# Optimization experiments

Measured on AMD Instinct MI355X. Metric: run time of the kernel, lower is better.

## Reference

```python
import jax, jax.numpy as jnp
import numpy as np

D_MODEL = 1024
D_INNER = 2048   # expand * d_model
D_STATE = 16
DT_RANK = 64     # ceil(d_model / 16)
D_CONV = 4
L = 2048
EPS = 1e-5


def setup_inputs() -> dict:
    key = jax.random.key(0)
    ks = jax.random.split(key, 8)
    sc = lambda k, shape: jax.random.normal(k, shape, jnp.float32) * 0.02
    A = jnp.tile(jnp.arange(1, D_STATE + 1, dtype=jnp.float32), (D_INNER, 1))
    return {
        "x": jax.random.normal(ks[0], (L, D_MODEL), jnp.float32),
        "W_in": sc(ks[1], (D_MODEL, 2 * D_INNER)),          # in_proj (no bias)
        "W_conv": sc(ks[2], (D_CONV, D_INNER)),             # depthwise conv kernel
        "b_conv": jnp.zeros((D_INNER,), jnp.float32),
        "W_x": sc(ks[3], (D_INNER, DT_RANK + 2 * D_STATE)), # x_proj (no bias)
        "W_dt": sc(ks[4], (DT_RANK, D_INNER)),
        "b_dt": jnp.zeros((D_INNER,), jnp.float32),
        "A_log": jnp.log(A),
        "D": jnp.ones((D_INNER,), jnp.float32),
        "W_out": sc(ks[5], (D_INNER, D_MODEL)),             # out_proj (no bias)
        "ln_scale": jnp.ones((D_MODEL,), jnp.float32),
        "ln_bias": jnp.zeros((D_MODEL,), jnp.float32),
        "drop_key": 0,  # unused: training=False -> DropPath is identity
    }


def reference(x, W_in, W_conv, b_conv, W_x, W_dt, b_dt, A_log, D, W_out,
              ln_scale, ln_bias, drop_key):
    l = x.shape[0]
    # LayerNorm (flax default: mean/var over features)
    mu = jnp.mean(x, axis=-1, keepdims=True)
    var = jnp.mean(jnp.square(x), axis=-1, keepdims=True) - jnp.square(mu)
    xn = (x - mu) * jax.lax.rsqrt(var + EPS) * ln_scale + ln_bias

    # MambaBlock
    xr = xn @ W_in                         # (l, 2*d_inner)
    u, res = xr[:, :D_INNER], xr[:, D_INNER:]

    # causal depthwise conv: pad left d_conv-1, take first l outputs
    up = jnp.pad(u, ((D_CONV - 1, 0), (0, 0)))
    uc = b_conv + sum(up[k:k + l] * W_conv[k] for k in range(D_CONV))
    u2 = jax.nn.silu(uc)                   # (l, d_inner)

    # SSM params (input-dependent)
    x_dbl = u2 @ W_x                       # (l, dt_rank + 2n)
    dt = x_dbl[:, :DT_RANK]
    B = x_dbl[:, DT_RANK:DT_RANK + D_STATE]
    C = x_dbl[:, DT_RANK + D_STATE:]
    delta = jax.nn.softplus(dt @ W_dt + b_dt)   # (l, d_inner)
    A = -jnp.exp(A_log)                         # (d_inner, n)

    dA = jnp.exp(jnp.einsum('ld,dn->ldn', delta, A))   # (l, d_inner, n)
    dBu = jnp.einsum('ld,ln->ldn', delta * u2, B)       # (l, d_inner, n)

    def step(h, inp):
        dA_t, dBu_t, C_t = inp
        h = dA_t * h + dBu_t               # (d_inner, n)
        return h, h @ C_t                  # y_t: (d_inner,)

    h0 = jnp.zeros((D_INNER, D_STATE), dtype=u2.dtype)
    _, ys = jax.lax.scan(step, h0, (dA, dBu, C))
    y = ys + u2 * D                        # (l, d_inner)

    y = y * jax.nn.silu(res)
    out = y @ W_out                        # (l, d_model)
    return out + x                         # residual (DropPath identity in eval)
```

## Files before the change

### kernel.cpp

```cpp
#include <hip/hip_runtime.h>
#include <math.h>

#define L_SEQ 2048
#define DM 1024
#define DI 2048
#define DS 16
#define DTR 64
#define EPS 1e-5f
#define NSEG 16
#define SEGLEN 128

typedef float f32x4 __attribute__((ext_vector_type(4)));
typedef __bf16 bf16x8 __attribute__((ext_vector_type(8)));
typedef _Float16 h16x4 __attribute__((ext_vector_type(4)));

static __device__ __forceinline__ unsigned short f2bf(float f) {
  union { float f; unsigned u; } v; v.f = f;
  unsigned r = v.u + 0x7fffu + ((v.u >> 16) & 1u);
  return (unsigned short)(r >> 16);
}
static __device__ __forceinline__ float bf2f(unsigned short s) {
  union { unsigned u; float f; } v; v.u = ((unsigned)s) << 16;
  return v.f;
}

static __device__ __forceinline__ void gload16(const void* g, void* l) {
  __builtin_amdgcn_global_load_lds(
      (__attribute__((address_space(1))) void*)(unsigned long long)(g),
      (__attribute__((address_space(3))) void*)(unsigned)(unsigned long long)(l),
      16, 0, 0);
}

__global__ __launch_bounds__(256) void ln_kernel(const float* __restrict__ x,
                                                 const float* __restrict__ sc,
                                                 const float* __restrict__ bi,
                                                 unsigned short* __restrict__ xnb) {
  int row = blockIdx.x;
  int t = threadIdx.x;
  float4 xv = ((const float4*)(x + (size_t)row * DM))[t];
  float s  = xv.x + xv.y + xv.z + xv.w;
  float s2 = xv.x*xv.x + xv.y*xv.y + xv.z*xv.z + xv.w*xv.w;
  #pragma unroll
  for (int m = 32; m >= 1; m >>= 1) {
    s  += __shfl_xor(s, m);
    s2 += __shfl_xor(s2, m);
  }
  __shared__ float red[8];
  int wid = t >> 6, lane = t & 63;
  if (lane == 0) { red[wid] = s; red[4 + wid] = s2; }
  __syncthreads();
  s  = red[0] + red[1] + red[2] + red[3];
  s2 = red[4] + red[5] + red[6] + red[7];
  float mu = s * (1.f / DM);
  float var = s2 * (1.f / DM) - mu * mu;
  float rs = rsqrtf(var + EPS);
  float4 sc4 = ((const float4*)sc)[t];
  float4 bi4 = ((const float4*)bi)[t];
  ushort4 ob;
  ob.x = f2bf((xv.x - mu) * rs * sc4.x + bi4.x);
  ob.y = f2bf((xv.y - mu) * rs * sc4.y + bi4.y);
  ob.z = f2bf((xv.z - mu) * rs * sc4.z + bi4.z);
  ob.w = f2bf((xv.w - mu) * rs * sc4.w + bi4.w);
  *(ushort4*)&xnb[(size_t)row * DM + t * 4] = ob;
}

__global__ __launch_bounds__(256) void trans_bf16(
    const float* __restrict__ W, unsigned short* __restrict__ Wt, int K, int N)
{
  __shared__ unsigned short s[64][80];
  int n0 = blockIdx.x * 64, k0 = blockIdx.y * 64;
  int tid = threadIdx.x;
  #pragma unroll
  for (int p = 0; p < 4; ++p) {
    int i = p * 16 + (tid >> 4);
    int j = (tid & 15) * 4;
    float4 w = *(const float4*)&W[(size_t)(k0 + i) * N + n0 + j];
    s[j + 0][i] = f2bf(w.x); s[j + 1][i] = f2bf(w.y);
    s[j + 2][i] = f2bf(w.z); s[j + 3][i] = f2bf(w.w);
  }
  __syncthreads();
  #pragma unroll
  for (int q = 0; q < 2; ++q) {
    int n = q * 32 + (tid >> 3);
    int i8 = (tid & 7) * 8;
    *(int4*)&Wt[(size_t)(n0 + n) * K + k0 + i8] = *(const int4*)&s[n][i8];
  }
}

__global__ __launch_bounds__(256) void transpose_b16(
    const unsigned short* __restrict__ in, unsigned short* __restrict__ out,
    int R, int C)
{
  __shared__ unsigned short s[64][72];
  int c0 = blockIdx.x * 64, r0 = blockIdx.y * 64;
  int tid = threadIdx.x;
  #pragma unroll
  for (int p = 0; p < 2; ++p) {
    int r = p * 32 + (tid >> 3);
    int c = (tid & 7) * 8;
    *(int4*)&s[r][c] = *(const int4*)&in[(size_t)(r0 + r) * C + c0 + c];
  }
  __syncthreads();
  #pragma unroll
  for (int p = 0; p < 2; ++p) {
    int c = p * 32 + (tid >> 3);
    int r = (tid & 7) * 8;
    ushort4 a, b;
    a.x = s[r + 0][c]; a.y = s[r + 1][c]; a.z = s[r + 2][c]; a.w = s[r + 3][c];
    b.x = s[r + 4][c]; b.y = s[r + 5][c]; b.z = s[r + 6][c]; b.w = s[r + 7][c];
    *(ushort4*)&out[(size_t)(c0 + c) * R + r0 + r] = a;
    *(ushort4*)&out[(size_t)(c0 + c) * R + r0 + r + 4] = b;
  }
}

__global__ __launch_bounds__(256) void trans_wx(
    const float* __restrict__ Wx, unsigned short* __restrict__ Wxt)
{
  int i = blockIdx.x * 256 + threadIdx.x;
  int n = i >> 11, k = i & 2047;
  Wxt[i] = (n < 96) ? f2bf(Wx[(size_t)k * 96 + n]) : (unsigned short)0;
}

template<int BM, int BN, int EPI, int OUTB, int SPLITK>
__global__ __launch_bounds__(256) void gemm2(
    const unsigned short* __restrict__ A, int lda,
    const unsigned short* __restrict__ Bt, int ldb,
    void* __restrict__ Cv, int ldc,
    int M, int N, int K,
    const float* __restrict__ bias)
{
  constexpr int WM = BM / 2, WN = BN / 2;
  constexpr int FM = WM / 16, FN = WN / 16;
  __shared__ __align__(16) unsigned short smA[BM * 64];
  __shared__ __align__(16) unsigned short smB[BN * 64];

  int nwg = gridDim.x * gridDim.y;
  int bid = blockIdx.y * gridDim.x + blockIdx.x;
  if ((nwg & 7) == 0) {
    int cpx = nwg >> 3;
    bid = (bid & 7) * cpx + (bid >> 3);
  }
  int bx = bid % gridDim.x;
  int by = bid / gridDim.x;
  int m0 = by * BM, n0 = bx * BN;

  int tid = threadIdx.x;
  int lane = tid & 63, wid = tid >> 6;
  int wm = wid >> 1, wn = wid & 1;

  int kb = blockIdx.z * (K / SPLITK);
  int nt = (K / SPLITK) / 64;

  int rs = lane >> 3;
  int cs = (lane & 7) * 8;

  f32x4 acc[FM][FN];
  #pragma unroll
  for (int m = 0; m < FM; ++m)
    #pragma unroll
    for (int n = 0; n < FN; ++n) acc[m][n] = (f32x4){0.f, 0.f, 0.f, 0.f};

  for (int kt = 0; kt < nt; ++kt) {
    __syncthreads();
    #pragma unroll
    for (int i = 0; i < BM / 32; ++i) {
      int chunk = wid * (BM / 32) + i;
      gload16(A + (size_t)(m0 + chunk * 8 + rs) * lda + kb + kt * 64 + cs,
              (char*)smA + chunk * 1024);
    }
    #pragma unroll
    for (int i = 0; i < BN / 32; ++i) {
      int chunk = wid * (BN / 32) + i;
      gload16(Bt + (size_t)(n0 + chunk * 8 + rs) * ldb + kb + kt * 64 + cs,
              (char*)smB + chunk * 1024);
    }
    __syncthreads();

    #pragma unroll
    for (int kk = 0; kk < 2; ++kk) {
      bf16x8 aF[FM], bF[FN];
      #pragma unroll
      for (int m = 0; m < FM; ++m) {
        int r = wm * WM + m * 16 + (lane & 15);
        aF[m] = *(const bf16x8*)((const char*)smA + r * 128 + kk * 64 + (lane >> 4) * 16);
      }
      #pragma unroll
      for (int n = 0; n < FN; ++n) {
        int r = wn * WN + n * 16 + (lane & 15);
        bF[n] = *(const bf16x8*)((const char*)smB + r * 128 + kk * 64 + (lane >> 4) * 16);
      }
      #pragma unroll
      for (int m = 0; m < FM; ++m)
        #pragma unroll
        for (int n = 0; n < FN; ++n)
          acc[m][n] = __builtin_amdgcn_mfma_f32_16x16x32_bf16(
              aF[m], bF[n], acc[m][n], 0, 0, 0);
    }
  }

  float* Cf = (float*)Cv + (size_t)blockIdx.z * M * ldc;
  unsigned short* Cb = (unsigned short*)Cv;
  int cm = (lane >> 4) * 4, cn = lane & 15;
  #pragma unroll
  for (int m = 0; m < FM; ++m)
    #pragma unroll
    for (int n = 0; n < FN; ++n) {
      int col = n0 + wn * WN + n * 16 + cn;
      #pragma unroll
      for (int r = 0; r < 4; ++r) {
        int row = m0 + wm * WM + m * 16 + cm + r;
        float v = acc[m][n][r];
        if (EPI == 1) {
          float w = v + bias[row];
          v = (w > 20.f) ? w : log1pf(__expf(w));
        }
        if (OUTB) Cb[(size_t)row * ldc + col] = f2bf(v);
        else      Cf[(size_t)row * ldc + col] = v;
      }
    }
}

__global__ __launch_bounds__(256) void xdbl_reduce(
    const float* __restrict__ part, unsigned short* __restrict__ xdbl)
{
  int i = (blockIdx.x * 256 + threadIdx.x) * 4;
  const int SL = 2048 * 128;
  float4 s = *(const float4*)&part[i];
  #pragma unroll
  for (int z = 1; z < 16; ++z) {
    float4 p = *(const float4*)&part[(size_t)z * SL + i];
    s.x += p.x; s.y += p.y; s.z += p.z; s.w += p.w;
  }
  ushort4 ob;
  ob.x = f2bf(s.x); ob.y = f2bf(s.y); ob.z = f2bf(s.z); ob.w = f2bf(s.w);
  *(ushort4*)&xdbl[i] = ob;
}

__global__ __launch_bounds__(256) void out_reduce(
    const float* __restrict__ part, const float* __restrict__ x,
    float* __restrict__ out)
{
  int i = (blockIdx.x * 256 + threadIdx.x) * 4;
  const int SL = 2048 * 1024;
  float4 a = *(const float4*)&part[i];
  float4 b = *(const float4*)&part[SL + i];
  float4 r = *(const float4*)&x[i];
  float4 o;
  o.x = a.x + b.x + r.x; o.y = a.y + b.y + r.y;
  o.z = a.z + b.z + r.z; o.w = a.w + b.w + r.w;
  *(float4*)&out[i] = o;
}

__global__ __launch_bounds__(256) void conv_silu_kernel(
    const unsigned short* __restrict__ xrT,
    const float* __restrict__ Wc, const float* __restrict__ bc,
    unsigned short* __restrict__ u2T)
{
  int d = blockIdx.x;
  int l0 = blockIdx.y * 1024 + threadIdx.x * 4;
  const unsigned short* ur = xrT + (size_t)d * L_SEQ;
  float w0 = Wc[0 * DI + d], w1 = Wc[1 * DI + d];
  float w2 = Wc[2 * DI + d], w3 = Wc[3 * DI + d];
  float b = bc[d];
  ushort4 v0 = *(const ushort4*)&ur[l0];
  ushort4 vm; vm.x = vm.y = vm.z = vm.w = 0;
  if (l0 > 0) vm = *(const ushort4*)&ur[l0 - 4];
  float um3 = bf2f(vm.y), um2 = bf2f(vm.z), um1 = bf2f(vm.w);
  float x0 = bf2f(v0.x), x1 = bf2f(v0.y), x2 = bf2f(v0.z), x3 = bf2f(v0.w);
  float y0 = b + w0 * um3 + w1 * um2 + w2 * um1 + w3 * x0;
  float y1 = b + w0 * um2 + w1 * um1 + w2 * x0  + w3 * x1;
  float y2 = b + w0 * um1 + w1 * x0  + w2 * x1  + w3 * x2;
  float y3 = b + w0 * x0  + w1 * x1  + w2 * x2  + w3 * x3;
  ushort4 ob;
  ob.x = f2bf(y0 / (1.f + __expf(-y0)));
  ob.y = f2bf(y1 / (1.f + __expf(-y1)));
  ob.z = f2bf(y2 / (1.f + __expf(-y2)));
  ob.w = f2bf(y3 / (1.f + __expf(-y3)));
  *(ushort4*)&u2T[(size_t)d * L_SEQ + l0] = ob;
}


__global__ __launch_bounds__(64) void scan_pass1(
    const unsigned short* __restrict__ deltaT, const unsigned short* __restrict__ u2T,
    const unsigned short* __restrict__ xdbl,
    const float* __restrict__ A_log,
    float* __restrict__ hend, float* __restrict__ aprod)
{
  int t = threadIdx.x;
  int ch = t >> 4, n = t & 15;
  int li = (t & 15) * 4;
  int d0 = blockIdx.x * 4, d = d0 + ch;
  int s = blockIdx.y;
  int base = s * SEGLEN;

  __shared__ __align__(16) float sdT[4][68], suT[4][68], sBT[16][68];

  float An = -__expf(A_log[d * DS + n]);
  float h = 0.f, P = 1.f;

  ushort4 rdu, ru, rB[4];
  auto LOAD = [&](int c0) {
    rdu = *(const ushort4*)&deltaT[(size_t)d * L_SEQ + c0 + li];
    ru  = *(const ushort4*)&u2T[(size_t)d * L_SEQ + c0 + li];
    #pragma unroll
    for (int r = 0; r < 4; ++r) {
      int ll = c0 + (t >> 2) + r * 16;
      rB[r] = *(const ushort4*)&xdbl[(size_t)ll * 128 + 64 + (t & 3) * 4];
    }
  };

  LOAD(base);
  for (int cc = 0; cc < 2; ++cc) {
    __syncthreads();
    sdT[ch][li + 0] = bf2f(rdu.x); sdT[ch][li + 1] = bf2f(rdu.y);
    sdT[ch][li + 2] = bf2f(rdu.z); sdT[ch][li + 3] = bf2f(rdu.w);
    suT[ch][li + 0] = bf2f(ru.x);  suT[ch][li + 1] = bf2f(ru.y);
    suT[ch][li + 2] = bf2f(ru.z);  suT[ch][li + 3] = bf2f(ru.w);
    #pragma unroll
    for (int r = 0; r < 4; ++r) {
      int ll = (t >> 2) + r * 16;
      int nb = (t & 3) * 4;
      sBT[nb + 0][ll] = bf2f(rB[r].x); sBT[nb + 1][ll] = bf2f(rB[r].y);
      sBT[nb + 2][ll] = bf2f(rB[r].z); sBT[nb + 3][ll] = bf2f(rB[r].w);
    }
    if (cc == 0) LOAD(base + 64);
    __syncthreads();

    #pragma unroll
    for (int g = 0; g < 64; g += 4) {
      float4 dl4 = *(const float4*)&sdT[ch][g];
      float4 ul4 = *(const float4*)&suT[ch][g];
      float4 Bn4 = *(const float4*)&sBT[n][g];
      float dl[4] = {dl4.x, dl4.y, dl4.z, dl4.w};
      float ul[4] = {ul4.x, ul4.y, ul4.z, ul4.w};
      float Bn[4] = {Bn4.x, Bn4.y, Bn4.z, Bn4.w};
      #pragma unroll
      for (int i = 0; i < 4; ++i) {
        float dA = __expf(dl[i] * An);
        P *= dA;
        h = dA * h + (dl[i] * ul[i]) * Bn[i];
      }
    }
  }
  size_t idx = (size_t)s * (DI * DS) + d0 * DS + t;
  hend[idx]  = h;
  aprod[idx] = P;
}

__global__ __launch_bounds__(64) void scan_pass3(
    const unsigned short* __restrict__ deltaT, const unsigned short* __restrict__ u2T,
    const unsigned short* __restrict__ resT,
    const unsigned short* __restrict__ xdbl,
    const float* __restrict__ A_log, const float* __restrict__ Dp,
    const float* __restrict__ hend, const float* __restrict__ aprod,
    unsigned short* __restrict__ ybT)
{
  int t = threadIdx.x;
  int ch = t >> 4, n = t & 15;
  int li = (t & 15) * 4;
  int d0 = blockIdx.x * 4, d = d0 + ch;
  int s = blockIdx.y;
  int base = s * SEGLEN;

  __shared__ __align__(16) float sdT[4][68], suT[4][68];
  __shared__ __align__(16) float sBT[16][68], sCT[16][68];
  __shared__ __align__(16) _Float16 svh[64][68];

  float An = -__expf(A_log[d * DS + n]);
  float Dd = Dp[d];

  float h = 0.f;
  int fi = d0 * DS + t;
  for (int k = 0; k < s; ++k)
    h = aprod[(size_t)k * (DI * DS) + fi] * h + hend[(size_t)k * (DI * DS) + fi];

  ushort4 rdu, ru, rB[4], rC[4];
  auto LOAD = [&](int c0) {
    rdu = *(const ushort4*)&deltaT[(size_t)d * L_SEQ + c0 + li];
    ru  = *(const ushort4*)&u2T[(size_t)d * L_SEQ + c0 + li];
    #pragma unroll
    for (int r = 0; r < 4; ++r) {
      int ll = c0 + (t >> 2) + r * 16;
      int n4 = (t & 3) * 4;
      rB[r] = *(const ushort4*)&xdbl[(size_t)ll * 128 + 64 + n4];
      rC[r] = *(const ushort4*)&xdbl[(size_t)ll * 128 + 80 + n4];
    }
  };

  LOAD(base);
  for (int cc = 0; cc < 2; ++cc) {
    int c0 = base + cc * 64;
    __syncthreads();
    sdT[ch][li + 0] = bf2f(rdu.x); sdT[ch][li + 1] = bf2f(rdu.y);
    sdT[ch][li + 2] = bf2f(rdu.z); sdT[ch][li + 3] = bf2f(rdu.w);
    suT[ch][li + 0] = bf2f(ru.x);  suT[ch][li + 1] = bf2f(ru.y);
    suT[ch][li + 2] = bf2f(ru.z);  suT[ch][li + 3] = bf2f(ru.w);
    #pragma unroll
    for (int r = 0; r < 4; ++r) {
      int ll = (t >> 2) + r * 16;
      int nb = (t & 3) * 4;
      sBT[nb + 0][ll] = bf2f(rB[r].x); sBT[nb + 1][ll] = bf2f(rB[r].y);
      sBT[nb + 2][ll] = bf2f(rB[r].z); sBT[nb + 3][ll] = bf2f(rB[r].w);
      sCT[nb + 0][ll] = bf2f(rC[r].x); sCT[nb + 1][ll] = bf2f(rC[r].y);
      sCT[nb + 2][ll] = bf2f(rC[r].z); sCT[nb + 3][ll] = bf2f(rC[r].w);
    }
    if (cc == 0) LOAD(base + 64);
    __syncthreads();

    #pragma unroll
    for (int g = 0; g < 64; g += 4) {
      float4 dl4 = *(const float4*)&sdT[ch][g];
      float4 ul4 = *(const float4*)&suT[ch][g];
      float4 Bn4 = *(const float4*)&sBT[n][g];
      float4 Cn4 = *(const float4*)&sCT[n][g];
      float dl[4] = {dl4.x, dl4.y, dl4.z, dl4.w};
      float ul[4] = {ul4.x, ul4.y, ul4.z, ul4.w};
      float Bn[4] = {Bn4.x, Bn4.y, Bn4.z, Bn4.w};
      float Cn[4] = {Cn4.x, Cn4.y, Cn4.z, Cn4.w};
      #pragma unroll
      for (int i = 0; i < 4; ++i) {
        float dA = __expf(dl[i] * An);
        h = dA * h + (dl[i] * ul[i]) * Bn[i];
        float vv = h * Cn[i];
        if (n == 0) vv += ul[i] * Dd;
        svh[g + i][t] = (_Float16)vv;
      }
    }
    __syncthreads();

    #pragma unroll
    for (int r = 0; r < 4; ++r) {
      int ll = (t >> 2) + r * 16;
      int c2 = t & 3;
      const h16x4* p = (const h16x4*)&svh[ll][c2 * 16];
      h16x4 a = p[0], b = p[1], c = p[2], e = p[3];
      float sA = ((float)a.x + (float)a.y) + ((float)a.z + (float)a.w);
      float sB = ((float)b.x + (float)b.y) + ((float)b.z + (float)b.w);
      float sC = ((float)c.x + (float)c.y) + ((float)c.z + (float)c.w);
      float sE = ((float)e.x + (float)e.y) + ((float)e.z + (float)e.w);
      float sum = (sA + sB) + (sC + sE);
      float rv = bf2f(resT[(size_t)(d0 + c2) * L_SEQ + c0 + ll]);
      float sig = 1.f / (1.f + __expf(-rv));
      ybT[(size_t)(d0 + c2) * L_SEQ + c0 + ll] = f2bf(sum * rv * sig);
    }
  }
}

extern "C" void kernel_launch(void* const* d_in, const int* in_sizes, int n_in,
                              void* d_out, int out_size, void* d_ws, size_t ws_size,
                              hipStream_t stream)
{
  const float* x      = (const float*)d_in[0];
  const float* W_in   = (const float*)d_in[1];
  const float* W_conv = (const float*)d_in[2];
  const float* b_conv = (const float*)d_in[3];
  const float* W_x    = (const float*)d_in[4];
  const float* W_dt   = (const float*)d_in[5];
  const float* b_dt   = (const float*)d_in[6];
  const float* A_log  = (const float*)d_in[7];
  const float* Dp     = (const float*)d_in[8];
  const float* W_out  = (const float*)d_in[9];
  const float* ln_s   = (const float*)d_in[10];
  const float* ln_b   = (const float*)d_in[11];

  char* ws = (char*)d_ws;
  const size_t MB = 1u << 20;
  unsigned short* xnb    = (unsigned short*)(ws);
  unsigned short* xrT    = (unsigned short*)(ws + 4 * MB);
  unsigned short* u2T    = (unsigned short*)(ws + 20 * MB);
  unsigned short* u2b    = (unsigned short*)(ws + 28 * MB);
  float*          hend   = (float*)(ws + 28 * MB);
  float*          aprod  = (float*)(ws + 30 * MB);
  unsigned short* xdbl   = (unsigned short*)(ws + 36 * MB);
  unsigned short* Wxt    = (unsigned short*)(ws + 36 * MB + 512 * 1024);
  unsigned short* Wdt_t  = (unsigned short*)(ws + 37 * MB);
  unsigned short* deltaTb= (unsigned short*)(ws + 38 * MB);
  unsigned short* Wtin   = (unsigned short*)(ws + 38 * MB);
  float*          part   = (float*)(ws + 46 * MB);
  unsigned short* ybT    = (unsigned short*)(ws + 54 * MB);
  unsigned short* yb     = (unsigned short*)(ws + 4 * MB);
  unsigned short* Wtout  = xnb;
  const unsigned short* resT = xrT + (size_t)DI * L_SEQ;

  ln_kernel<<<L_SEQ, 256, 0, stream>>>(x, ln_s, ln_b, xnb);

  trans_bf16<<<dim3((2 * DI) / 64, DM / 64), 256, 0, stream>>>(W_in, Wtin, DM, 2 * DI);

  gemm2<64, 128, 0, 1, 1><<<dim3(L_SEQ / 128, (2 * DI) / 64), 256, 0, stream>>>(
      Wtin, DM, xnb, DM, xrT, L_SEQ, 2 * DI, L_SEQ, DM, nullptr);

  conv_silu_kernel<<<dim3(DI, 2), 256, 0, stream>>>(xrT, W_conv, b_conv, u2T);

  transpose_b16<<<dim3(L_SEQ / 64, DI / 64), 256, 0, stream>>>(u2T, u2b, DI, L_SEQ);

  trans_wx<<<(128 * 2048) / 256, 256, 0, stream>>>(W_x, Wxt);

  gemm2<64, 128, 0, 0, 16><<<dim3(1, L_SEQ / 64, 16), 256, 0, stream>>>(
      u2b, DI, Wxt, DI, part, 128, L_SEQ, 128, DI, nullptr);

  xdbl_reduce<<<(L_SEQ * 128) / 1024, 256, 0, stream>>>(part, xdbl);

  trans_bf16<<<dim3(DI / 64, DTR / 64), 256, 0, stream>>>(W_dt, Wdt_t, DTR, DI);

  gemm2<64, 128, 1, 1, 1><<<dim3(L_SEQ / 128, DI / 64), 256, 0, stream>>>(
      Wdt_t, DTR, xdbl, 128, deltaTb, L_SEQ, DI, L_SEQ, DTR, b_dt);

  trans_bf16<<<dim3(DM / 64, DI / 64), 256, 0, stream>>>(W_out, Wtout, DI, DM);

  scan_pass1<<<dim3(DI / 4, NSEG), 64, 0, stream>>>(
      deltaTb, u2T, xdbl, A_log, hend, aprod);

  scan_pass3<<<dim3(DI / 4, NSEG), 64, 0, stream>>>(
      deltaTb, u2T, resT, xdbl, A_log, Dp, hend, aprod, ybT);

  transpose_b16<<<dim3(L_SEQ / 64, DI / 64), 256, 0, stream>>>(ybT, yb, DI, L_SEQ);

  gemm2<64, 64, 0, 0, 2><<<dim3(DM / 64, L_SEQ / 64, 2), 256, 0, stream>>>(
      yb, DI, Wtout, DI, part, DM, L_SEQ, DM, DI, nullptr);

  out_reduce<<<(L_SEQ * DM) / 1024, 256, 0, stream>>>(part, x, (float*)d_out);
}
```

Measured before the change: 189.0 us.

## Widen scan blocks to 8 channels, precompute delta*u, skip last segment pass1

Both scan kernels now run 128-thread blocks covering 8 channels instead of 4, so each block loads the shared B/C tiles once for twice as many channels. The delta*u product is computed once per element while staging to shared memory rather than per state lane. The D skip term moves from the inner loop into the final reduction, and pass1 no longer launches for the last segment, whose end state is never consumed. The wider shared staging buffer and re-read of u2 add some shared memory and global traffic per block.

Result: faster. 185.2 us (-2.0%).

```diff
diff --git a/kernel.cpp b/kernel.cpp
--- a/kernel.cpp
+++ b/kernel.cpp
@@ -12,7 +12,7 @@
 
 typedef float f32x4 __attribute__((ext_vector_type(4)));
 typedef __bf16 bf16x8 __attribute__((ext_vector_type(8)));
-typedef _Float16 h16x4 __attribute__((ext_vector_type(4)));
+typedef _Float16 h16x2 __attribute__((ext_vector_type(2)));
 
 static __device__ __forceinline__ unsigned short f2bf(float f) {
   union { float f; unsigned u; } v; v.f = f;
@@ -280,7 +280,7 @@
 }
 
 
-__global__ __launch_bounds__(64) void scan_pass1(
+__global__ __launch_bounds__(128) void scan_pass1(
     const unsigned short* __restrict__ deltaT, const unsigned short* __restrict__ u2T,
     const unsigned short* __restrict__ xdbl,
     const float* __restrict__ A_log,
@@ -289,39 +289,40 @@
   int t = threadIdx.x;
   int ch = t >> 4, n = t & 15;
   int li = (t & 15) * 4;
-  int d0 = blockIdx.x * 4, d = d0 + ch;
+  int d0 = blockIdx.x * 8, d = d0 + ch;
   int s = blockIdx.y;
   int base = s * SEGLEN;
 
-  __shared__ __align__(16) float sdT[4][68], suT[4][68], sBT[16][68];
+  __shared__ __align__(16) float sdT[8][68], suT[8][68], sBT[16][68];
 
   float An = -__expf(A_log[d * DS + n]);
   float h = 0.f, P = 1.f;
 
-  ushort4 rdu, ru, rB[4];
+  ushort4 rdu, ru, rB[2];
   auto LOAD = [&](int c0) {
     rdu = *(const ushort4*)&deltaT[(size_t)d * L_SEQ + c0 + li];
     ru  = *(const ushort4*)&u2T[(size_t)d * L_SEQ + c0 + li];
     #pragma unroll
-    for (int r = 0; r < 4; ++r) {
-      int ll = c0 + (t >> 2) + r * 16;
-      rB[r] = *(const ushort4*)&xdbl[(size_t)ll * 128 + 64 + (t & 3) * 4];
+    for (int q = 0; q < 2; ++q) {
+      int ll = c0 + (t >> 2) + q * 32;
+      rB[q] = *(const ushort4*)&xdbl[(size_t)ll * 128 + 64 + (t & 3) * 4];
     }
   };
 
   LOAD(base);
   for (int cc = 0; cc < 2; ++cc) {
     __syncthreads();
-    sdT[ch][li + 0] = bf2f(rdu.x); sdT[ch][li + 1] = bf2f(rdu.y);
-    sdT[ch][li + 2] = bf2f(rdu.z); sdT[ch][li + 3] = bf2f(rdu.w);
-    suT[ch][li + 0] = bf2f(ru.x);  suT[ch][li + 1] = bf2f(ru.y);
-    suT[ch][li + 2] = bf2f(ru.z);  suT[ch][li + 3] = bf2f(ru.w);
-    #pragma unroll
-    for (int r = 0; r < 4; ++r) {
-      int ll = (t >> 2) + r * 16;
+    float d0v = bf2f(rdu.x), d1v = bf2f(rdu.y), d2v = bf2f(rdu.z), d3v = bf2f(rdu.w);
+    sdT[ch][li + 0] = d0v; sdT[ch][li + 1] = d1v;
+    sdT[ch][li + 2] = d2v; sdT[ch][li + 3] = d3v;
+    suT[ch][li + 0] = d0v * bf2f(ru.x); suT[ch][li + 1] = d1v * bf2f(ru.y);
+    suT[ch][li + 2] = d2v * bf2f(ru.z); suT[ch][li + 3] = d3v * bf2f(ru.w);
+    #pragma unroll
+    for (int q = 0; q < 2; ++q) {
+      int ll = (t >> 2) + q * 32;
       int nb = (t & 3) * 4;
-      sBT[nb + 0][ll] = bf2f(rB[r].x); sBT[nb + 1][ll] = bf2f(rB[r].y);
-      sBT[nb + 2][ll] = bf2f(rB[r].z); sBT[nb + 3][ll] = bf2f(rB[r].w);
+      sBT[nb + 0][ll] = bf2f(rB[q].x); sBT[nb + 1][ll] = bf2f(rB[q].y);
+      sBT[nb + 2][ll] = bf2f(rB[q].z); sBT[nb + 3][ll] = bf2f(rB[q].w);
     }
     if (cc == 0) LOAD(base + 64);
     __syncthreads();
@@ -329,16 +330,16 @@
     #pragma unroll
     for (int g = 0; g < 64; g += 4) {
       float4 dl4 = *(const float4*)&sdT[ch][g];
-      float4 ul4 = *(const float4*)&suT[ch][g];
+      float4 du4 = *(const float4*)&suT[ch][g];
       float4 Bn4 = *(const float4*)&sBT[n][g];
       float dl[4] = {dl4.x, dl4.y, dl4.z, dl4.w};
-      float ul[4] = {ul4.x, ul4.y, ul4.z, ul4.w};
+      float du[4] = {du4.x, du4.y, du4.z, du4.w};
       float Bn[4] = {Bn4.x, Bn4.y, Bn4.z, Bn4.w};
       #pragma unroll
       for (int i = 0; i < 4; ++i) {
         float dA = __expf(dl[i] * An);
         P *= dA;
-        h = dA * h + (dl[i] * ul[i]) * Bn[i];
+        h = dA * h + du[i] * Bn[i];
       }
     }
   }
@@ -347,7 +348,7 @@
   aprod[idx] = P;
 }
 
-__global__ __launch_bounds__(64) void scan_pass3(
+__global__ __launch_bounds__(128) void scan_pass3(
     const unsigned short* __restrict__ deltaT, const unsigned short* __restrict__ u2T,
     const unsigned short* __restrict__ resT,
     const unsigned short* __restrict__ xdbl,
@@ -358,32 +359,31 @@
   int t = threadIdx.x;
   int ch = t >> 4, n = t & 15;
   int li = (t & 15) * 4;
-  int d0 = blockIdx.x * 4, d = d0 + ch;
+  int d0 = blockIdx.x * 8, d = d0 + ch;
   int s = blockIdx.y;
   int base = s * SEGLEN;
 
-  __shared__ __align__(16) float sdT[4][68], suT[4][68];
+  __shared__ __align__(16) float sdT[8][68], suT[8][68];
   __shared__ __align__(16) float sBT[16][68], sCT[16][68];
-  __shared__ __align__(16) _Float16 svh[64][68];
+  __shared__ __align__(4) _Float16 svh[64][134];
 
   float An = -__expf(A_log[d * DS + n]);
-  float Dd = Dp[d];
 
   float h = 0.f;
   int fi = d0 * DS + t;
   for (int k = 0; k < s; ++k)
     h = aprod[(size_t)k * (DI * DS) + fi] * h + hend[(size_t)k * (DI * DS) + fi];
 
-  ushort4 rdu, ru, rB[4], rC[4];
+  ushort4 rdu, ru, rB[2], rC[2];
   auto LOAD = [&](int c0) {
     rdu = *(const ushort4*)&deltaT[(size_t)d * L_SEQ + c0 + li];
     ru  = *(const ushort4*)&u2T[(size_t)d * L_SEQ + c0 + li];
     #pragma unroll
-    for (int r = 0; r < 4; ++r) {
-      int ll = c0 + (t >> 2) + r * 16;
+    for (int q = 0; q < 2; ++q) {
+      int ll = c0 + (t >> 2) + q * 32;
       int n4 = (t & 3) * 4;
-      rB[r] = *(const ushort4*)&xdbl[(size_t)ll * 128 + 64 + n4];
-      rC[r] = *(const ushort4*)&xdbl[(size_t)ll * 128 + 80 + n4];
+      rB[q] = *(const ushort4*)&xdbl[(size_t)ll * 128 + 64 + n4];
+      rC[q] = *(const ushort4*)&xdbl[(size_t)ll * 128 + 80 + n4];
     }
   };
 
@@ -391,18 +391,19 @@
   for (int cc = 0; cc < 2; ++cc) {
     int c0 = base + cc * 64;
     __syncthreads();
-    sdT[ch][li + 0] = bf2f(rdu.x); sdT[ch][li + 1] = bf2f(rdu.y);
-    sdT[ch][li + 2] = bf2f(rdu.z); sdT[ch][li + 3] = bf2f(rdu.w);
-    suT[ch][li + 0] = bf2f(ru.x);  suT[ch][li + 1] = bf2f(ru.y);
-    suT[ch][li + 2] = bf2f(ru.z);  suT[ch][li + 3] = bf2f(ru.w);
-    #pragma unroll
-    for (int r = 0; r < 4; ++r) {
-      int ll = (t >> 2) + r * 16;
+    float d0v = bf2f(rdu.x), d1v = bf2f(rdu.y), d2v = bf2f(rdu.z), d3v = bf2f(rdu.w);
+    sdT[ch][li + 0] = d0v; sdT[ch][li + 1] = d1v;
+    sdT[ch][li + 2] = d2v; sdT[ch][li + 3] = d3v;
+    suT[ch][li + 0] = d0v * bf2f(ru.x); suT[ch][li + 1] = d1v * bf2f(ru.y);
+    suT[ch][li + 2] = d2v * bf2f(ru.z); suT[ch][li + 3] = d3v * bf2f(ru.w);
+    #pragma unroll
+    for (int q = 0; q < 2; ++q) {
+      int ll = (t >> 2) + q * 32;
       int nb = (t & 3) * 4;
-      sBT[nb + 0][ll] = bf2f(rB[r].x); sBT[nb + 1][ll] = bf2f(rB[r].y);
-      sBT[nb + 2][ll] = bf2f(rB[r].z); sBT[nb + 3][ll] = bf2f(rB[r].w);
-      sCT[nb + 0][ll] = bf2f(rC[r].x); sCT[nb + 1][ll] = bf2f(rC[r].y);
-      sCT[nb + 2][ll] = bf2f(rC[r].z); sCT[nb + 3][ll] = bf2f(rC[r].w);
+      sBT[nb + 0][ll] = bf2f(rB[q].x); sBT[nb + 1][ll] = bf2f(rB[q].y);
+      sBT[nb + 2][ll] = bf2f(rB[q].z); sBT[nb + 3][ll] = bf2f(rB[q].w);
+      sCT[nb + 0][ll] = bf2f(rC[q].x); sCT[nb + 1][ll] = bf2f(rC[q].y);
+      sCT[nb + 2][ll] = bf2f(rC[q].z); sCT[nb + 3][ll] = bf2f(rC[q].w);
     }
     if (cc == 0) LOAD(base + 64);
     __syncthreads();
@@ -410,38 +411,39 @@
     #pragma unroll
     for (int g = 0; g < 64; g += 4) {
       float4 dl4 = *(const float4*)&sdT[ch][g];
-      float4 ul4 = *(const float4*)&suT[ch][g];
+      float4 du4 = *(const float4*)&suT[ch][g];
       float4 Bn4 = *(const float4*)&sBT[n][g];
       float4 Cn4 = *(const float4*)&sCT[n][g];
       float dl[4] = {dl4.x, dl4.y, dl4.z, dl4.w};
-      float ul[4] = {ul4.x, ul4.y, ul4.z, ul4.w};
+      float du[4] = {du4.x, du4.y, du4.z, du4.w};
       float Bn[4] = {Bn4.x, Bn4.y, Bn4.z, Bn4.w};
       float Cn[4] = {Cn4.x, Cn4.y, Cn4.z, Cn4.w};
       #pragma unroll
       for (int i = 0; i < 4; ++i) {
         float dA = __expf(dl[i] * An);
-        h = dA * h + (dl[i] * ul[i]) * Bn[i];
-        float vv = h * Cn[i];
-        if (n == 0) vv += ul[i] * Dd;
-        svh[g + i][t] = (_Float16)vv;
+        h = dA * h + du[i] * Bn[i];
+        svh[g + i][t] = (_Float16)(h * Cn[i]);
       }
     }
     __syncthreads();
 
     #pragma unroll
     for (int r = 0; r < 4; ++r) {
-      int ll = (t >> 2) + r * 16;
-      int c2 = t & 3;
-      const h16x4* p = (const h16x4*)&svh[ll][c2 * 16];
-      h16x4 a = p[0], b = p[1], c = p[2], e = p[3];
-      float sA = ((float)a.x + (float)a.y) + ((float)a.z + (float)a.w);
-      float sB = ((float)b.x + (float)b.y) + ((float)b.z + (float)b.w);
-      float sC = ((float)c.x + (float)c.y) + ((float)c.z + (float)c.w);
-      float sE = ((float)e.x + (float)e.y) + ((float)e.z + (float)e.w);
-      float sum = (sA + sB) + (sC + sE);
-      float rv = bf2f(resT[(size_t)(d0 + c2) * L_SEQ + c0 + ll]);
+      int idx = r * 128 + t;
+      int ll = idx & 63, c2 = idx >> 6;
+      const _Float16* row = &svh[ll][c2 * 16];
+      float sum = 0.f;
+      #pragma unroll
+      for (int k = 0; k < 8; ++k) {
+        h16x2 pv = *(const h16x2*)&row[k * 2];
+        sum += (float)pv.x + (float)pv.y;
+      }
+      int dd = d0 + c2;
+      float uv = bf2f(u2T[(size_t)dd * L_SEQ + c0 + ll]);
+      float rv = bf2f(resT[(size_t)dd * L_SEQ + c0 + ll]);
       float sig = 1.f / (1.f + __expf(-rv));
-      ybT[(size_t)(d0 + c2) * L_SEQ + c0 + ll] = f2bf(sum * rv * sig);
+      float yv = (sum + uv * Dp[dd]) * rv * sig;
+      ybT[(size_t)dd * L_SEQ + c0 + ll] = f2bf(yv);
     }
   }
 }
@@ -507,10 +509,10 @@
 
   trans_bf16<<<dim3(DM / 64, DI / 64), 256, 0, stream>>>(W_out, Wtout, DI, DM);
 
-  scan_pass1<<<dim3(DI / 4, NSEG), 64, 0, stream>>>(
+  scan_pass1<<<dim3(DI / 8, NSEG - 1), 128, 0, stream>>>(
       deltaTb, u2T, xdbl, A_log, hend, aprod);
 
-  scan_pass3<<<dim3(DI / 4, NSEG), 64, 0, stream>>>(
+  scan_pass3<<<dim3(DI / 8, NSEG), 128, 0, stream>>>(
       deltaTb, u2T, resT, xdbl, A_log, Dp, hend, aprod, ybT);
 
   transpose_b16<<<dim3(L_SEQ / 64, DI / 64), 256, 0, stream>>>(ybT, yb, DI, L_SEQ);
```
